# Kernel optimization log

Hardware: AMD Instinct MI355X
Metric: run time of the kernel (lower is better)

The kernel has to match this reference:

```python
import jax, jax.numpy as jnp
import numpy as np

B, K, D = 4, 4096, 2048

def setup_inputs() -> dict:
    key = jax.random.key(0)
    k1, k2, k3 = jax.random.split(key, 3)
    x = jax.random.normal(k1, (B, K, D), dtype=jnp.float32)
    # Conv1d(dim, dim, kernel_size=1) weight [D, D, 1] squeezed to a dense [D_out, D_in] matrix
    W = jax.random.normal(k2, (D, D), dtype=jnp.float32) / np.sqrt(D)
    b = jax.random.normal(k3, (D,), dtype=jnp.float32) * 0.02
    return {"x": x, "W": W, "b": b}

def reference(x, W, b):
    # lam_t = sigmoid(dt_proj(u_t)); pointwise conv1d == per-timestep linear
    lam = jax.nn.sigmoid(jnp.einsum("bkd,ed->bke", x, W) + b)  # [B,K,D]
    # Gated linear recurrence: s_t = lam_t * s_{t-1} + (1 - lam_t) * u_t
    def step(s, inp):
        lam_t, u_t = inp  # each [B,D]
        s = lam_t * s + (1.0 - lam_t) * u_t
        return s, s
    s0 = jnp.zeros((x.shape[0], x.shape[2]), dtype=x.dtype)
    _, ys = jax.lax.scan(step, s0, (jnp.moveaxis(lam, 1, 0), jnp.moveaxis(x, 1, 0)))
    return jnp.moveaxis(ys, 0, 1)  # [B,K,D]
```

## Files before the change

kernel.cpp:

```cpp
#include <hip/hip_runtime.h>
#include <hip/hip_bf16.h>

#define B_SZ 4
#define K_SEQ 4096
#define D_DIM 2048
#define M_ROWS (B_SZ * K_SEQ)

#define CHUNK 32
#define NCHUNK (K_SEQ / CHUNK)

typedef __attribute__((ext_vector_type(8))) short short8;
typedef __attribute__((ext_vector_type(4))) float floatx4;
typedef __attribute__((ext_vector_type(8))) unsigned short ushortx8;

__device__ __forceinline__ unsigned short f2bf_rne(float f) {
  unsigned int u = __float_as_uint(f);
  u += 0x7fffu + ((u >> 16) & 1u);
  return (unsigned short)(u >> 16);
}
__device__ __forceinline__ float bf2f(unsigned short u) {
  return __uint_as_float(((unsigned int)u) << 16);
}

#define NX4 (M_ROWS * D_DIM / 4)
#define NW4 (D_DIM * D_DIM / 4)
__global__ void cvt_bf16_kernel(const float* __restrict__ x,
                                const float* __restrict__ W,
                                unsigned short* __restrict__ xb,
                                unsigned short* __restrict__ Wb) {
  int i = blockIdx.x * blockDim.x + threadIdx.x;
  const float* src;
  unsigned short* dst;
  int j;
  if (i < NX4) { src = x; dst = xb; j = i; }
  else         { src = W; dst = Wb; j = i - NX4; }
  float4 v = ((const float4*)src)[j];
  ushort4 o;
  o.x = f2bf_rne(v.x);
  o.y = f2bf_rne(v.y);
  o.z = f2bf_rne(v.z);
  o.w = f2bf_rne(v.w);
  ((ushort4*)dst)[j] = o;
}

__device__ __forceinline__ void gl_lds16(const void* g, void* l) {
  __builtin_amdgcn_global_load_lds(
      (const __attribute__((address_space(1))) unsigned int*)g,
      (__attribute__((address_space(3))) unsigned int*)l, 16, 0, 0);
}

#define WAITVM_(n) asm volatile("s_waitcnt vmcnt(" #n ")" ::: "memory")
#define WAITVM(n) WAITVM_(n)

template <bool GBF>
__global__ __launch_bounds__(512, 2)
void gemm8_kernel(const unsigned short* __restrict__ Ag,
                  const unsigned short* __restrict__ Wg,
                  const float* __restrict__ bias,
                  void* __restrict__ lamv) {
  __shared__ __align__(16) unsigned short smem[65536];

  const int tid = threadIdx.x;
  const int lane = tid & 63;
  const int wave = tid >> 6;
  const int wr = wave >> 2;
  const int wc = wave & 3;
  const int bm = (blockIdx.x >> 3) * 256;
  const int bn = (blockIdx.x & 7) * 256;

  const int lane15 = lane & 15;
  const int tA = (wr == 0) ? 0 : 3;
  const int tB = (wc < 2) ? 1 : 2;
  const int sw16 = ((lane >> 2) & 1) << 4;
  const int kg8 = (lane >> 4) << 3;
  const int rA15 = lane15 * 64 + (kg8 ^ sw16);
  const int bb15 = ((wc & 1) << 12) + rA15;

  const int r_s = tid >> 3;
  const int lcol = (((tid & 7) ^ (((tid >> 5) & 1) << 1)) << 3);
  const unsigned short* gA0p = Ag + (size_t)(bm + r_s) * D_DIM + lcol;
  const unsigned short* gA1p = Ag + (size_t)(bm + 128 + r_s) * D_DIM + lcol;
  const unsigned short* gB0p = Wg + (size_t)(bn + r_s) * D_DIM + lcol;
  const unsigned short* gB1p = Wg + (size_t)(bn + 128 + r_s) * D_DIM + lcol;
  const int st8 = tid * 8;

#define STG(T, gp, jt)                                                        \
  {                                                                           \
    unsigned short* d_ = smem + (((T) + (((jt) & 1) << 2)) << 13) + st8;      \
    const unsigned short* s_ = (gp) + ((size_t)(jt) << 6);                    \
    gl_lds16(s_, d_);                                                         \
    gl_lds16(s_ + 64 * (size_t)D_DIM, d_ + 4096);                             \
  }

  floatx4 acc[8][4];
#pragma unroll
  for (int i = 0; i < 8; ++i)
#pragma unroll
    for (int j = 0; j < 4; ++j)
      acc[i][j] = (floatx4){0.f, 0.f, 0.f, 0.f};

#define MFMA16(AB, AF, BF)                                                    \
  _Pragma("unroll") for (int mf = 0; mf < 4; ++mf)                            \
  _Pragma("unroll") for (int nf = 0; nf < 4; ++nf)                            \
      acc[(AB) + mf][nf] = __builtin_amdgcn_mfma_f32_16x16x32_bf16(           \
          AF[mf], BF[nf], acc[(AB) + mf][nf], 0, 0, 0);

  STG(0, gA0p, 0);
  STG(1, gB0p, 0);
  STG(3, gA1p, 0);
  STG(2, gB1p, 0);
  STG(0, gA0p, 1);
  WAITVM(2);
  __builtin_amdgcn_s_barrier();

#define TILE(j, DOS1, DOS2, DOS4, V4)                                         \
  {                                                                           \
    const unsigned short* pA =                                                \
        smem + ((tA + (((j) & 1) << 2)) << 13) + rA15;                        \
    const unsigned short* pB =                                                \
        smem + ((tB + (((j) & 1) << 2)) << 13) + bb15;                        \
    short8 a0k0[4], a0k1[4], a1k0[4], a1k1[4], bk0[4], bk1[4];                \
                         \
    _Pragma("unroll") for (int mf = 0; mf < 4; ++mf) {                        \
      a0k0[mf] = *(const short8*)(pA + mf * 1024);                            \
      a0k1[mf] = *(const short8*)(pA + mf * 1024 + 32);                       \
    }                                                                         \
    _Pragma("unroll") for (int nf = 0; nf < 4; ++nf)                          \
        bk0[nf] = *(const short8*)(pB + nf * 1024);                           \
    if (DOS1) { STG(1, gB0p, (j) + 1); STG(3, gA1p, (j) + 1); }               \
    __builtin_amdgcn_s_barrier();                                             \
    asm volatile("s_waitcnt lgkmcnt(0)" ::: "memory");                        \
    __builtin_amdgcn_sched_barrier(0);                                        \
    __builtin_amdgcn_s_setprio(1);                                            \
    MFMA16(0, a0k0, bk0);                                                     \
    __builtin_amdgcn_s_setprio(0);                                            \
                                 \
    _Pragma("unroll") for (int mf = 0; mf < 4; ++mf) {                        \
      a1k0[mf] = *(const short8*)(pA + 4096 + mf * 1024);                     \
      a1k1[mf] = *(const short8*)(pA + 4096 + mf * 1024 + 32);                \
    }                                                                         \
    if (DOS2) { STG(2, gB1p, (j) + 1); }                                      \
    __builtin_amdgcn_s_barrier();                                             \
    asm volatile("s_waitcnt lgkmcnt(0)" ::: "memory");                        \
    __builtin_amdgcn_sched_barrier(0);                                        \
    __builtin_amdgcn_s_setprio(1);                                            \
    MFMA16(4, a1k0, bk0);                                                     \
    __builtin_amdgcn_s_setprio(0);                                            \
                                              \
    _Pragma("unroll") for (int nf = 0; nf < 4; ++nf)                          \
        bk1[nf] = *(const short8*)(pB + nf * 1024 + 32);                      \
    __builtin_amdgcn_s_barrier();                                             \
    asm volatile("s_waitcnt lgkmcnt(0)" ::: "memory");                        \
    __builtin_amdgcn_sched_barrier(0);                                        \
    __builtin_amdgcn_s_setprio(1);                                            \
    MFMA16(4, a1k1, bk1);                                                     \
    __builtin_amdgcn_s_setprio(0);                                            \
          \
          \
    if (DOS4) { STG(0, gA0p, (j) + 2); }                                      \
    if ((V4) == 2) { WAITVM(2); }                                             \
    else if ((V4) == 0) { WAITVM(0); }                                        \
    __builtin_amdgcn_s_barrier();                                             \
    asm volatile("s_waitcnt lgkmcnt(0)" ::: "memory");                        \
    __builtin_amdgcn_sched_barrier(0);                                        \
    __builtin_amdgcn_s_setprio(1);                                            \
    MFMA16(0, a0k1, bk1);                                                     \
    __builtin_amdgcn_s_setprio(0);                                            \
  }

#pragma unroll 2
  for (int j = 0; j < 30; ++j) TILE(j, 1, 1, 1, 2);
  TILE(30, 1, 1, 0, 0);
  TILE(31, 0, 0, 0, -1);
#undef TILE
#undef STG
#undef MFMA16

  const int crow = (lane >> 4) << 2;
#pragma unroll
  for (int nf = 0; nf < 4; ++nf) {
    const int ge = bn + wc * 64 + nf * 16 + lane15;
    const float bb = bias[ge];
#pragma unroll
    for (int mf = 0; mf < 8; ++mf) {
      const int gm0 = bm + wr * 128 + mf * 16 + crow;
#pragma unroll
      for (int r = 0; r < 4; ++r) {
        float v = acc[mf][nf][r] + bb;
        size_t off = (size_t)(gm0 + r) * D_DIM + ge;
        if constexpr (GBF) {
          float g = 1.0f / (1.0f + __expf(v));
          ((unsigned short*)lamv)[off] = f2bf_rne(g);
        } else {
          ((float*)lamv)[off] = 1.0f / (1.0f + __expf(-v));
        }
      }
    }
  }
}


__global__ void scan_reduce_bf(const unsigned short* __restrict__ gb,
                               const unsigned short* __restrict__ xb,
                               float* __restrict__ Ach,
                               float* __restrict__ Bch) {
  int idx = blockIdx.x * blockDim.x + threadIdx.x;
  int d8 = idx & 255;
  int c = (idx >> 8) & (NCHUNK - 1);
  int b = idx >> 15;
  size_t base = ((size_t)(b * K_SEQ + c * CHUNK)) * D_DIM + d8 * 8;
  float A[8], Bv[8];
#pragma unroll
  for (int j = 0; j < 8; ++j) { A[j] = 1.f; Bv[j] = 0.f; }
#pragma unroll 8
  for (int t = 0; t < CHUNK; ++t) {
    size_t o = base + (size_t)t * D_DIM;
    ushortx8 g8 = *(const ushortx8*)(gb + o);
    ushortx8 u8 = *(const ushortx8*)(xb + o);
#pragma unroll
    for (int j = 0; j < 8; ++j) {
      float g = bf2f(g8[j]), u = bf2f(u8[j]);
      A[j] -= g * A[j];
      Bv[j] += g * (u - Bv[j]);
    }
  }
  float4 a0 = make_float4(A[0], A[1], A[2], A[3]);
  float4 a1 = make_float4(A[4], A[5], A[6], A[7]);
  float4 b0 = make_float4(Bv[0], Bv[1], Bv[2], Bv[3]);
  float4 b1 = make_float4(Bv[4], Bv[5], Bv[6], Bv[7]);
  ((float4*)Ach)[idx * 2] = a0;
  ((float4*)Ach)[idx * 2 + 1] = a1;
  ((float4*)Bch)[idx * 2] = b0;
  ((float4*)Bch)[idx * 2 + 1] = b1;
}

__global__ void scan_prefix_kernel(const float* __restrict__ Ach,
                                   const float* __restrict__ Bch,
                                   float* __restrict__ Sst) {
  int idx = blockIdx.x * blockDim.x + threadIdx.x;
  int d4 = idx & (D_DIM / 4 - 1);
  int b = idx >> 9;
  float4 s = make_float4(0.f, 0.f, 0.f, 0.f);
#pragma unroll 4
  for (int c = 0; c < NCHUNK; ++c) {
    int o4 = (b * NCHUNK + c) * (D_DIM / 4) + d4;
    ((float4*)Sst)[o4] = s;
    float4 A = ((const float4*)Ach)[o4];
    float4 Bv = ((const float4*)Bch)[o4];
    s.x = A.x * s.x + Bv.x;
    s.y = A.y * s.y + Bv.y;
    s.z = A.z * s.z + Bv.z;
    s.w = A.w * s.w + Bv.w;
  }
}

__global__ void scan_apply_bf(const unsigned short* __restrict__ gb,
                              const unsigned short* __restrict__ xb,
                              const float* __restrict__ Sst,
                              float* __restrict__ out) {
  int idx = blockIdx.x * blockDim.x + threadIdx.x;
  int d8 = idx & 255;
  int c = (idx >> 8) & (NCHUNK - 1);
  int b = idx >> 15;
  size_t base = ((size_t)(b * K_SEQ + c * CHUNK)) * D_DIM + d8 * 8;
  float4 s0 = ((const float4*)Sst)[idx * 2];
  float4 s1 = ((const float4*)Sst)[idx * 2 + 1];
  float s[8] = {s0.x, s0.y, s0.z, s0.w, s1.x, s1.y, s1.z, s1.w};
#pragma unroll 8
  for (int t = 0; t < CHUNK; ++t) {
    size_t o = base + (size_t)t * D_DIM;
    ushortx8 g8 = *(const ushortx8*)(gb + o);
    ushortx8 u8 = *(const ushortx8*)(xb + o);
#pragma unroll
    for (int j = 0; j < 8; ++j) {
      float g = bf2f(g8[j]), u = bf2f(u8[j]);
      s[j] += g * (u - s[j]);
    }
    *(float4*)(out + o) = make_float4(s[0], s[1], s[2], s[3]);
    *(float4*)(out + o + 4) = make_float4(s[4], s[5], s[6], s[7]);
  }
}

__global__ void scan_reduce_kernel(const float* __restrict__ lam,
                                   const unsigned short* __restrict__ xb,
                                   float* __restrict__ Ach,
                                   float* __restrict__ Bch) {
  int idx = blockIdx.x * blockDim.x + threadIdx.x;
  int d4 = idx & (D_DIM / 4 - 1);
  int c = (idx >> 9) & (NCHUNK - 1);
  int b = idx >> 16;
  size_t base = ((size_t)(b * K_SEQ + c * CHUNK)) * D_DIM + d4 * 4;
  float4 Aacc = make_float4(1.f, 1.f, 1.f, 1.f);
  float4 Bv = make_float4(0.f, 0.f, 0.f, 0.f);
#pragma unroll 4
  for (int t = 0; t < CHUNK; ++t) {
    size_t o = base + (size_t)t * D_DIM;
    float4 l = *(const float4*)(lam + o);
    ushort4 ub = *(const ushort4*)(xb + o);
    Aacc.x *= l.x; Bv.x = l.x * (Bv.x - bf2f(ub.x)) + bf2f(ub.x);
    Aacc.y *= l.y; Bv.y = l.y * (Bv.y - bf2f(ub.y)) + bf2f(ub.y);
    Aacc.z *= l.z; Bv.z = l.z * (Bv.z - bf2f(ub.z)) + bf2f(ub.z);
    Aacc.w *= l.w; Bv.w = l.w * (Bv.w - bf2f(ub.w)) + bf2f(ub.w);
  }
  ((float4*)Ach)[idx] = Aacc;
  ((float4*)Bch)[idx] = Bv;
}

__global__ void scan_apply_kernel(float* lamout,
                                  const unsigned short* __restrict__ xb,
                                  const float* __restrict__ Sst) {
  int idx = blockIdx.x * blockDim.x + threadIdx.x;
  int d4 = idx & (D_DIM / 4 - 1);
  int c = (idx >> 9) & (NCHUNK - 1);
  int b = idx >> 16;
  size_t base = ((size_t)(b * K_SEQ + c * CHUNK)) * D_DIM + d4 * 4;
  float4 s = ((const float4*)Sst)[idx];
#pragma unroll 4
  for (int t = 0; t < CHUNK; ++t) {
    size_t o = base + (size_t)t * D_DIM;
    float4 l = *(const float4*)(lamout + o);
    ushort4 ub = *(const ushort4*)(xb + o);
    s.x = l.x * (s.x - bf2f(ub.x)) + bf2f(ub.x);
    s.y = l.y * (s.y - bf2f(ub.y)) + bf2f(ub.y);
    s.z = l.z * (s.z - bf2f(ub.z)) + bf2f(ub.z);
    s.w = l.w * (s.w - bf2f(ub.w)) + bf2f(ub.w);
    *(float4*)(lamout + o) = s;
  }
}

extern "C" void kernel_launch(void* const* d_in, const int* in_sizes, int n_in,
                              void* d_out, int out_size, void* d_ws, size_t ws_size,
                              hipStream_t stream) {
  const float* x = (const float*)d_in[0];
  const float* W = (const float*)d_in[1];
  const float* bias = (const float*)d_in[2];
  float* out = (float*)d_out;

  char* ws = (char*)d_ws;
  const size_t NEED_BF = 148897792ULL;
  const bool bfpath = (ws_size >= NEED_BF);

  unsigned short* x_bf = (unsigned short*)ws;
  unsigned short* W_bf = (unsigned short*)(ws + 67108864ULL);

  cvt_bf16_kernel<<<(NX4 + NW4) / 256, 256, 0, stream>>>(x, W, x_bf, W_bf);

  dim3 ggrid((M_ROWS / 256) * (D_DIM / 256));

  if (bfpath) {
    unsigned short* g_bf = (unsigned short*)(ws + 75497472ULL);
    float* Ach = (float*)(ws + 67108864ULL);
    float* Bch = (float*)(ws + 71303168ULL);
    float* Sst = (float*)(ws + 142606336ULL);

    gemm8_kernel<true><<<ggrid, 512, 0, stream>>>(x_bf, W_bf, bias, g_bf);

    int total8 = B_SZ * NCHUNK * D_DIM / 8;
    scan_reduce_bf<<<total8 / 256, 256, 0, stream>>>(g_bf, x_bf, Ach, Bch);
    scan_prefix_kernel<<<(B_SZ * D_DIM / 4) / 256, 256, 0, stream>>>(Ach, Bch, Sst);
    scan_apply_bf<<<total8 / 256, 256, 0, stream>>>(g_bf, x_bf, Sst, out);
  } else {
    float* Ach = (float*)(ws + 75497472ULL);
    float* Bch = (float*)(ws + 79691776ULL);
    float* Sst = (float*)(ws + 83886080ULL);

    gemm8_kernel<false><<<ggrid, 512, 0, stream>>>(x_bf, W_bf, bias, out);

    int total4 = B_SZ * NCHUNK * D_DIM / 4;
    scan_reduce_kernel<<<total4 / 256, 256, 0, stream>>>(out, x_bf, Ach, Bch);
    scan_prefix_kernel<<<(B_SZ * D_DIM / 4) / 256, 256, 0, stream>>>(Ach, Bch, Sst);
    scan_apply_kernel<<<total4 / 256, 256, 0, stream>>>(out, x_bf, Sst);
  }
}
```

Before: 439.6 us.

## Use full XOR LDS swizzle in GEMM and double scan chunk length

The GEMM's LDS layout moves from a 2-way XOR swizzle to a full 8-way XOR swizzle over 16-byte columns, in both the global-to-LDS store and the fragment reads. This is meant to remove LDS bank conflicts on the MFMA operand loads. The scan chunk length doubles from 32 to 64, which halves the chunk-summary traffic, and the prefix kernel switches from float4 to one scalar per thread to keep enough threads in flight. The cost is that the reduce and apply kernels launch half as many threads, each running a longer serial loop.

```diff
diff --git a/kernel.cpp b/kernel.cpp
--- a/kernel.cpp
+++ b/kernel.cpp
@@ -6,7 +6,7 @@
 #define D_DIM 2048
 #define M_ROWS (B_SZ * K_SEQ)
 
-#define CHUNK 32
+#define CHUNK 64
 #define NCHUNK (K_SEQ / CHUNK)
 
 typedef __attribute__((ext_vector_type(8))) short short8;
@@ -71,13 +71,14 @@
   const int lane15 = lane & 15;
   const int tA = (wr == 0) ? 0 : 3;
   const int tB = (wc < 2) ? 1 : 2;
-  const int sw16 = ((lane >> 2) & 1) << 4;
+  const int swz = (lane15 & 7) << 3;
   const int kg8 = (lane >> 4) << 3;
-  const int rA15 = lane15 * 64 + (kg8 ^ sw16);
-  const int bb15 = ((wc & 1) << 12) + rA15;
+  const int k0off = kg8 ^ swz;
+  const int k1off = k0off ^ 32;
+  const int rowoff = lane15 * 64;
 
   const int r_s = tid >> 3;
-  const int lcol = (((tid & 7) ^ (((tid >> 5) & 1) << 1)) << 3);
+  const int lcol = (((tid & 7) ^ ((tid >> 3) & 7)) << 3);
   const unsigned short* gA0p = Ag + (size_t)(bm + r_s) * D_DIM + lcol;
   const unsigned short* gA1p = Ag + (size_t)(bm + 128 + r_s) * D_DIM + lcol;
   const unsigned short* gB0p = Wg + (size_t)(bn + r_s) * D_DIM + lcol;
@@ -116,17 +117,17 @@
 #define TILE(j, DOS1, DOS2, DOS4, V4)                                         \
   {                                                                           \
     const unsigned short* pA =                                                \
-        smem + ((tA + (((j) & 1) << 2)) << 13) + rA15;                        \
+        smem + ((tA + (((j) & 1) << 2)) << 13) + rowoff;                      \
     const unsigned short* pB =                                                \
-        smem + ((tB + (((j) & 1) << 2)) << 13) + bb15;                        \
+        smem + ((tB + (((j) & 1) << 2)) << 13) + ((wc & 1) << 12) + rowoff;   \
     short8 a0k0[4], a0k1[4], a1k0[4], a1k1[4], bk0[4], bk1[4];                \
                          \
     _Pragma("unroll") for (int mf = 0; mf < 4; ++mf) {                        \
-      a0k0[mf] = *(const short8*)(pA + mf * 1024);                            \
-      a0k1[mf] = *(const short8*)(pA + mf * 1024 + 32);                       \
+      a0k0[mf] = *(const short8*)(pA + mf * 1024 + k0off);                    \
+      a0k1[mf] = *(const short8*)(pA + mf * 1024 + k1off);                    \
     }                                                                         \
     _Pragma("unroll") for (int nf = 0; nf < 4; ++nf)                          \
-        bk0[nf] = *(const short8*)(pB + nf * 1024);                           \
+        bk0[nf] = *(const short8*)(pB + nf * 1024 + k0off);                   \
     if (DOS1) { STG(1, gB0p, (j) + 1); STG(3, gA1p, (j) + 1); }               \
     __builtin_amdgcn_s_barrier();                                             \
     asm volatile("s_waitcnt lgkmcnt(0)" ::: "memory");                        \
@@ -136,8 +137,8 @@
     __builtin_amdgcn_s_setprio(0);                                            \
                                  \
     _Pragma("unroll") for (int mf = 0; mf < 4; ++mf) {                        \
-      a1k0[mf] = *(const short8*)(pA + 4096 + mf * 1024);                     \
-      a1k1[mf] = *(const short8*)(pA + 4096 + mf * 1024 + 32);                \
+      a1k0[mf] = *(const short8*)(pA + 4096 + mf * 1024 + k0off);             \
+      a1k1[mf] = *(const short8*)(pA + 4096 + mf * 1024 + k1off);             \
     }                                                                         \
     if (DOS2) { STG(2, gB1p, (j) + 1); }                                      \
     __builtin_amdgcn_s_barrier();                                             \
@@ -148,7 +149,7 @@
     __builtin_amdgcn_s_setprio(0);                                            \
                                               \
     _Pragma("unroll") for (int nf = 0; nf < 4; ++nf)                          \
-        bk1[nf] = *(const short8*)(pB + nf * 1024 + 32);                      \
+        bk1[nf] = *(const short8*)(pB + nf * 1024 + k1off);                   \
     __builtin_amdgcn_s_barrier();                                             \
     asm volatile("s_waitcnt lgkmcnt(0)" ::: "memory");                        \
     __builtin_amdgcn_sched_barrier(0);                                        \
@@ -207,7 +208,7 @@
   int idx = blockIdx.x * blockDim.x + threadIdx.x;
   int d8 = idx & 255;
   int c = (idx >> 8) & (NCHUNK - 1);
-  int b = idx >> 15;
+  int b = idx >> 14;
   size_t base = ((size_t)(b * K_SEQ + c * CHUNK)) * D_DIM + d8 * 8;
   float A[8], Bv[8];
 #pragma unroll
@@ -238,19 +239,14 @@
                                    const float* __restrict__ Bch,
                                    float* __restrict__ Sst) {
   int idx = blockIdx.x * blockDim.x + threadIdx.x;
-  int d4 = idx & (D_DIM / 4 - 1);
-  int b = idx >> 9;
-  float4 s = make_float4(0.f, 0.f, 0.f, 0.f);
+  int d = idx & (D_DIM - 1);
+  int b = idx >> 11;
+  float s = 0.f;
 #pragma unroll 4
   for (int c = 0; c < NCHUNK; ++c) {
-    int o4 = (b * NCHUNK + c) * (D_DIM / 4) + d4;
-    ((float4*)Sst)[o4] = s;
-    float4 A = ((const float4*)Ach)[o4];
-    float4 Bv = ((const float4*)Bch)[o4];
-    s.x = A.x * s.x + Bv.x;
-    s.y = A.y * s.y + Bv.y;
-    s.z = A.z * s.z + Bv.z;
-    s.w = A.w * s.w + Bv.w;
+    int o = (b * NCHUNK + c) * D_DIM + d;
+    Sst[o] = s;
+    s = Ach[o] * s + Bch[o];
   }
 }
 
@@ -261,7 +257,7 @@
   int idx = blockIdx.x * blockDim.x + threadIdx.x;
   int d8 = idx & 255;
   int c = (idx >> 8) & (NCHUNK - 1);
-  int b = idx >> 15;
+  int b = idx >> 14;
   size_t base = ((size_t)(b * K_SEQ + c * CHUNK)) * D_DIM + d8 * 8;
   float4 s0 = ((const float4*)Sst)[idx * 2];
   float4 s1 = ((const float4*)Sst)[idx * 2 + 1];
@@ -288,7 +284,7 @@
   int idx = blockIdx.x * blockDim.x + threadIdx.x;
   int d4 = idx & (D_DIM / 4 - 1);
   int c = (idx >> 9) & (NCHUNK - 1);
-  int b = idx >> 16;
+  int b = idx >> 15;
   size_t base = ((size_t)(b * K_SEQ + c * CHUNK)) * D_DIM + d4 * 4;
   float4 Aacc = make_float4(1.f, 1.f, 1.f, 1.f);
   float4 Bv = make_float4(0.f, 0.f, 0.f, 0.f);
@@ -312,7 +308,7 @@
   int idx = blockIdx.x * blockDim.x + threadIdx.x;
   int d4 = idx & (D_DIM / 4 - 1);
   int c = (idx >> 9) & (NCHUNK - 1);
-  int b = idx >> 16;
+  int b = idx >> 15;
   size_t base = ((size_t)(b * K_SEQ + c * CHUNK)) * D_DIM + d4 * 4;
   float4 s = ((const float4*)Sst)[idx];
 #pragma unroll 4
@@ -357,7 +353,7 @@
 
     int total8 = B_SZ * NCHUNK * D_DIM / 8;
     scan_reduce_bf<<<total8 / 256, 256, 0, stream>>>(g_bf, x_bf, Ach, Bch);
-    scan_prefix_kernel<<<(B_SZ * D_DIM / 4) / 256, 256, 0, stream>>>(Ach, Bch, Sst);
+    scan_prefix_kernel<<<(B_SZ * D_DIM) / 256, 256, 0, stream>>>(Ach, Bch, Sst);
     scan_apply_bf<<<total8 / 256, 256, 0, stream>>>(g_bf, x_bf, Sst, out);
   } else {
     float* Ach = (float*)(ws + 75497472ULL);
@@ -368,7 +364,7 @@
 
     int total4 = B_SZ * NCHUNK * D_DIM / 4;
     scan_reduce_kernel<<<total4 / 256, 256, 0, stream>>>(out, x_bf, Ach, Bch);
-    scan_prefix_kernel<<<(B_SZ * D_DIM / 4) / 256, 256, 0, stream>>>(Ach, Bch, Sst);
+    scan_prefix_kernel<<<(B_SZ * D_DIM) / 256, 256, 0, stream>>>(Ach, Bch, Sst);
     scan_apply_kernel<<<total4 / 256, 256, 0, stream>>>(out, x_bf, Sst);
   }
 }
```

Result: no change. 434.9 us (-1.0%).
